# Performance work log

Hardware: AMD Instinct MI355X
Metric: run time of the kernel (lower is better)

Reference implementation:

```python
import jax, jax.numpy as jnp
import numpy as np

NUM_HEADS = 16


def setup_inputs() -> dict:
    key = jax.random.key(0)
    k1, k2, k3 = jax.random.split(key, 3)
    B, L, H = 2, 2048, 1024
    return {
        "key": jax.random.normal(k1, (B, L, H), dtype=jnp.float32),
        "W_ctx": jax.random.normal(k2, (H, H), dtype=jnp.float32) * (1.0 / np.sqrt(H)),
        "b_ctx": jax.random.normal(k3, (H,), dtype=jnp.float32) * 0.01,
    }


def reference(key, W_ctx, b_ctx):
    # Note: the torch module defines q/k/v Linear layers but never calls them
    # in forward(); it reshapes the raw input into heads directly.
    B, L, H = key.shape
    dh = H // NUM_HEADS
    # [B, L, H] -> [B, nh, L, dh]
    x = key.reshape(B, L, NUM_HEADS, dh).transpose(0, 2, 1, 3)
    # QK^T then scale by sqrt(head_dim) (key.shape[-1] after head split)
    scores = jnp.einsum("bhqd,bhkd->bhqk", x, x) * (1.0 / np.float32(np.sqrt(dh)))
    attn = jax.nn.softmax(scores, axis=-1)  # dropout p treated as eval/identity
    ctx = jnp.einsum("bhqk,bhkd->bhqd", attn, x)
    # [B, nh, L, dh] -> [B, L, H]
    ctx = ctx.transpose(0, 2, 1, 3).reshape(B, L, H)
    # context_transform: nn.Linear(H, H, bias=True)
    return ctx @ W_ctx.T + b_ctx
```

## Files before the change

kernel.cpp:

```cpp
#include <hip/hip_runtime.h>
#include <stdint.h>

#define NH     16
#define LSEQ   2048
#define DH     64
#define HDIM   1024
#define BATCH  2

typedef __attribute__((ext_vector_type(8))) short bf16x8;
typedef __attribute__((ext_vector_type(4))) short bf16x4;
typedef __attribute__((ext_vector_type(8))) unsigned short u16x8;
typedef __attribute__((ext_vector_type(4))) float f32x4;

static __device__ inline unsigned short f2bs(float f) {
    union { float f; uint32_t u; } v; v.f = f;
    uint32_t u = v.u;
    return (unsigned short)((u + 0x7FFFu + ((u >> 16) & 1u)) >> 16);
}

#define GLOAD_LDS(gp, lp) \
    __builtin_amdgcn_global_load_lds((const __attribute__((address_space(1))) void*)(gp), \
                                     (__attribute__((address_space(3))) void*)(lp), 16, 0, 0)

#define QK_SCALE 0.42466083f

__global__ __launch_bounds__(256) void prep_kernel(const float* __restrict__ x,
                                                   const float* __restrict__ W,
                                                   unsigned short* __restrict__ xb,
                                                   unsigned short* __restrict__ xt,
                                                   unsigned short* __restrict__ wbt) {
    const int lt = blockIdx.x, bh = blockIdx.y;
    const int bid = bh * 32 + lt;
    const int t = threadIdx.x;

    if (t < 128) {
        const int gid = bid * 128 + t;
        const int n  = gid >> 7;
        const int kc = gid & 127;
        const float* src = W + (size_t)n * 1024 + kc * 8;
        float4 f0 = *(const float4*)(src);
        float4 f1 = *(const float4*)(src + 4);
        u16x8 v;
        v[0]=f2bs(f0.x); v[1]=f2bs(f0.y); v[2]=f2bs(f0.z); v[3]=f2bs(f0.w);
        v[4]=f2bs(f1.x); v[5]=f2bs(f1.y); v[6]=f2bs(f1.z); v[7]=f2bs(f1.w);
        const int nt = n >> 7, rn = n & 127;
        const int kt = kc >> 3, c = kc & 7;
        *(u16x8*)(wbt + (((size_t)nt * 16 + kt) * 128 + rn) * 64 + ((c ^ (rn & 7)) * 8)) = v;
    }

    const int b = bh >> 4, h = bh & 15;
    const int r = t >> 2, cp = t & 3;

    __shared__ __align__(16) unsigned short Sm[64][72];

    const float* src = x + ((size_t)(b * LSEQ + lt * 64 + r)) * HDIM + h * DH + cp * 16;
    float4 f0 = *(const float4*)(src);
    float4 f1 = *(const float4*)(src + 4);
    float4 f2 = *(const float4*)(src + 8);
    float4 f3 = *(const float4*)(src + 12);
    u16x8 lo, hi;
    lo[0]=f2bs(f0.x); lo[1]=f2bs(f0.y); lo[2]=f2bs(f0.z); lo[3]=f2bs(f0.w);
    lo[4]=f2bs(f1.x); lo[5]=f2bs(f1.y); lo[6]=f2bs(f1.z); lo[7]=f2bs(f1.w);
    hi[0]=f2bs(f2.x); hi[1]=f2bs(f2.y); hi[2]=f2bs(f2.z); hi[3]=f2bs(f2.w);
    hi[4]=f2bs(f3.x); hi[5]=f2bs(f3.y); hi[6]=f2bs(f3.z); hi[7]=f2bs(f3.w);
    u16x8 slo, shi;
    slo[0]=f2bs(f0.x*QK_SCALE); slo[1]=f2bs(f0.y*QK_SCALE); slo[2]=f2bs(f0.z*QK_SCALE); slo[3]=f2bs(f0.w*QK_SCALE);
    slo[4]=f2bs(f1.x*QK_SCALE); slo[5]=f2bs(f1.y*QK_SCALE); slo[6]=f2bs(f1.z*QK_SCALE); slo[7]=f2bs(f1.w*QK_SCALE);
    shi[0]=f2bs(f2.x*QK_SCALE); shi[1]=f2bs(f2.y*QK_SCALE); shi[2]=f2bs(f2.z*QK_SCALE); shi[3]=f2bs(f2.w*QK_SCALE);
    shi[4]=f2bs(f3.x*QK_SCALE); shi[5]=f2bs(f3.y*QK_SCALE); shi[6]=f2bs(f3.z*QK_SCALE); shi[7]=f2bs(f3.w*QK_SCALE);

    {
        unsigned short* kt = xb + ((size_t)bid) * 4096;
        const int s  = r >> 4, rla = r & 15;
        const int ks = cp >> 1, q0 = (cp & 1) * 2;
        *(u16x8*)(kt + ((s * 2 + ks) * 64 + q0 * 16 + rla) * 8)       = slo;
        *(u16x8*)(kt + ((s * 2 + ks) * 64 + (q0 + 1) * 16 + rla) * 8) = shi;
    }
    *(u16x8*)&Sm[r][cp * 16]     = lo;
    *(u16x8*)&Sm[r][cp * 16 + 8] = hi;
    __syncthreads();

    {
        const int dt = t >> 6, lane = t & 63;
        const int la = lane & 15, quad = lane >> 4;
        const int sw = (lane >> 2) & 3;
        unsigned short* vt = xt + ((size_t)bid) * 4096;
        unsigned short* row = vt + (dt * 64 + lane) * 16;
        #pragma unroll
        for (int g = 0; g < 4; ++g) {
            ushort4 fr;
            fr.x = Sm[g * 16 + quad * 4 + 0][dt * 16 + la];
            fr.y = Sm[g * 16 + quad * 4 + 1][dt * 16 + la];
            fr.z = Sm[g * 16 + quad * 4 + 2][dt * 16 + la];
            fr.w = Sm[g * 16 + quad * 4 + 3][dt * 16 + la];
            *(ushort4*)(row + ((g ^ sw) * 4)) = fr;
        }
    }
}

__global__ __launch_bounds__(256) void attn_kernel(const unsigned short* __restrict__ xb,
                                                   const unsigned short* __restrict__ xt,
                                                   unsigned short* __restrict__ ctxt) {
    const int bh = blockIdx.x;
    const int qt = blockIdx.y;
    const int tid = threadIdx.x;
    const int w = tid >> 6, lane = tid & 63;
    const int la = lane & 15, quad = lane >> 4;
    const int vsw = (lane >> 2) & 3;

    __shared__ __align__(16) unsigned short KL[2][4096];
    __shared__ __align__(16) unsigned short VL[2][4096];

    const unsigned short* xbh = xb + (size_t)bh * 32 * 4096;
    const unsigned short* xth = xt + (size_t)bh * 32 * 4096;
    const int qbase = qt * 128 + w * 32;

    bf16x8 qf[2][2];
    {
        const unsigned short* qs = xbh + (qbase >> 6) * 4096 + ((qbase >> 4) & 3) * 1024;
        qf[0][0] = *(const bf16x8*)(qs + lane * 8);
        qf[0][1] = *(const bf16x8*)(qs + 512 + lane * 8);
        qf[1][0] = *(const bf16x8*)(qs + 1024 + lane * 8);
        qf[1][1] = *(const bf16x8*)(qs + 1536 + lane * 8);
    }

    const f32x4 fzero = {0.f, 0.f, 0.f, 0.f};
    f32x4 acc0[4], acc1[4];
    #pragma unroll
    for (int j = 0; j < 4; ++j) { acc0[j] = fzero; acc1[j] = fzero; }
    float lp0 = 0.f, lp1 = 0.f;

    const int soff = tid * 16;
    #pragma unroll
    for (int j = 0; j < 2; ++j) {
        const int off = j * 4096 + soff;
        GLOAD_LDS((const char*)xbh + off, (char*)KL[0] + off);
        GLOAD_LDS((const char*)xth + off, (char*)VL[0] + off);
    }
    __syncthreads();

    const char* kp = (const char*)xbh + 8192;
    const char* vp = (const char*)xth + 8192;

    for (int tt = 0; tt < 32; ++tt) {
        if (tt < 31) {
            char* kdst = (char*)KL[(tt + 1) & 1];
            GLOAD_LDS(kp + soff,        kdst + soff);
            GLOAD_LDS(kp + 4096 + soff, kdst + 4096 + soff);
        }

        const unsigned short* kb = KL[tt & 1];
        bf16x4 pf0[4], pf1[4];
        {
            float ls0 = 0.f, ls1 = 0.f;
            #pragma unroll
            for (int kvt = 0; kvt < 4; ++kvt) {
                bf16x8 kf0 = *(const bf16x8*)(kb + (kvt * 2 + 0) * 512 + lane * 8);
                bf16x8 kf1 = *(const bf16x8*)(kb + (kvt * 2 + 1) * 512 + lane * 8);
                f32x4 s0 = fzero, s1 = fzero;
                s0 = __builtin_amdgcn_mfma_f32_16x16x32_bf16(kf0, qf[0][0], s0, 0, 0, 0);
                s0 = __builtin_amdgcn_mfma_f32_16x16x32_bf16(kf1, qf[0][1], s0, 0, 0, 0);
                s1 = __builtin_amdgcn_mfma_f32_16x16x32_bf16(kf0, qf[1][0], s1, 0, 0, 0);
                s1 = __builtin_amdgcn_mfma_f32_16x16x32_bf16(kf1, qf[1][1], s1, 0, 0, 0);

                {
                    float p0 = __builtin_amdgcn_exp2f(s0[0]);
                    float p1 = __builtin_amdgcn_exp2f(s0[1]);
                    float p2 = __builtin_amdgcn_exp2f(s0[2]);
                    float p3 = __builtin_amdgcn_exp2f(s0[3]);
                    ls0 += (p0 + p1) + (p2 + p3);
                    union { uint2 u; bf16x4 v; } cv;
                    cv.u = make_uint2(
                        __builtin_amdgcn_perm(__float_as_uint(p1), __float_as_uint(p0), 0x07060302),
                        __builtin_amdgcn_perm(__float_as_uint(p3), __float_as_uint(p2), 0x07060302));
                    pf0[kvt] = cv.v;
                }
                {
                    float p0 = __builtin_amdgcn_exp2f(s1[0]);
                    float p1 = __builtin_amdgcn_exp2f(s1[1]);
                    float p2 = __builtin_amdgcn_exp2f(s1[2]);
                    float p3 = __builtin_amdgcn_exp2f(s1[3]);
                    ls1 += (p0 + p1) + (p2 + p3);
                    union { uint2 u; bf16x4 v; } cv;
                    cv.u = make_uint2(
                        __builtin_amdgcn_perm(__float_as_uint(p1), __float_as_uint(p0), 0x07060302),
                        __builtin_amdgcn_perm(__float_as_uint(p3), __float_as_uint(p2), 0x07060302));
                    pf1[kvt] = cv.v;
                }
            }
            lp0 += ls0;
            lp1 += ls1;
        }

        __syncthreads();

        if (tt < 31) {
            char* vdst = (char*)VL[(tt + 1) & 1];
            GLOAD_LDS(vp + soff,        vdst + soff);
            GLOAD_LDS(vp + 4096 + soff, vdst + 4096 + soff);
            kp += 8192;
            vp += 8192;
        }

        const unsigned short* vb = VL[tt & 1];
        #pragma unroll
        for (int dt = 0; dt < 4; ++dt) {
            const unsigned short* vrow = vb + (dt * 64 + lane) * 16;
            bf16x4 vf0 = *(const bf16x4*)(vrow + ((0 ^ vsw) * 4));
            bf16x4 vf1 = *(const bf16x4*)(vrow + ((1 ^ vsw) * 4));
            bf16x4 vf2 = *(const bf16x4*)(vrow + ((2 ^ vsw) * 4));
            bf16x4 vf3 = *(const bf16x4*)(vrow + ((3 ^ vsw) * 4));
            f32x4 a0 = acc0[dt], a1 = acc1[dt];
            a0 = __builtin_amdgcn_mfma_f32_16x16x16bf16_1k(vf0, pf0[0], a0, 0, 0, 0);
            a0 = __builtin_amdgcn_mfma_f32_16x16x16bf16_1k(vf1, pf0[1], a0, 0, 0, 0);
            a0 = __builtin_amdgcn_mfma_f32_16x16x16bf16_1k(vf2, pf0[2], a0, 0, 0, 0);
            a0 = __builtin_amdgcn_mfma_f32_16x16x16bf16_1k(vf3, pf0[3], a0, 0, 0, 0);
            a1 = __builtin_amdgcn_mfma_f32_16x16x16bf16_1k(vf0, pf1[0], a1, 0, 0, 0);
            a1 = __builtin_amdgcn_mfma_f32_16x16x16bf16_1k(vf1, pf1[1], a1, 0, 0, 0);
            a1 = __builtin_amdgcn_mfma_f32_16x16x16bf16_1k(vf2, pf1[2], a1, 0, 0, 0);
            a1 = __builtin_amdgcn_mfma_f32_16x16x16bf16_1k(vf3, pf1[3], a1, 0, 0, 0);
            acc0[dt] = a0;
            acc1[dt] = a1;
        }
    }

    const int b = bh >> 4, h = bh & 15;
    const int mt = b * 16 + qt;
    unsigned short* tbase = ctxt + ((size_t)mt * 16 + h) * 128 * 64;
    {
        float l0 = lp0;
        l0 += __shfl_xor(l0, 16);
        l0 += __shfl_xor(l0, 32);
        float l1 = lp1;
        l1 += __shfl_xor(l1, 16);
        l1 += __shfl_xor(l1, 32);
        const float inv0 = 1.0f / l0;
        const float inv1 = 1.0f / l1;

        const int rr0 = w * 32 + la;
        unsigned short* rowp0 = tbase + rr0 * 64 + (quad & 1) * 4;
        #pragma unroll
        for (int dt = 0; dt < 4; ++dt) {
            f32x4 a = acc0[dt];
            const int c = dt * 2 + (quad >> 1);
            *(ushort4*)(rowp0 + ((c ^ (rr0 & 7)) * 8)) =
                make_ushort4(f2bs(a[0] * inv0), f2bs(a[1] * inv0),
                             f2bs(a[2] * inv0), f2bs(a[3] * inv0));
        }
        const int rr1 = w * 32 + 16 + la;
        unsigned short* rowp1 = tbase + rr1 * 64 + (quad & 1) * 4;
        #pragma unroll
        for (int dt = 0; dt < 4; ++dt) {
            f32x4 a = acc1[dt];
            const int c = dt * 2 + (quad >> 1);
            *(ushort4*)(rowp1 + ((c ^ (rr1 & 7)) * 8)) =
                make_ushort4(f2bs(a[0] * inv1), f2bs(a[1] * inv1),
                             f2bs(a[2] * inv1), f2bs(a[3] * inv1));
        }
    }
}

__global__ __launch_bounds__(256) void proj_kernel(const unsigned short* __restrict__ ctxt,
                                                   const unsigned short* __restrict__ wbt,
                                                   const float* __restrict__ bias,
                                                   float* __restrict__ out) {
    const int ntb = blockIdx.x;
    const int mtb = blockIdx.y;
    const int tid = threadIdx.x;
    const int w = tid >> 6, lane = tid & 63;
    const int la = lane & 15, quad = lane >> 4;
    const int wm = (w >> 1) * 64, wn = (w & 1) * 64;

    __shared__ __align__(16) unsigned short As[2][8192];
    __shared__ __align__(16) unsigned short Bs[2][8192];

    const unsigned short* abase = ctxt + (size_t)mtb * 16 * 8192;
    const unsigned short* bbase = wbt  + (size_t)ntb * 16 * 8192;

    const int sw0 = ((quad)     ^ (la & 7)) * 8;
    const int sw1 = ((quad + 4) ^ (la & 7)) * 8;

    const f32x4 fzero = {0.f, 0.f, 0.f, 0.f};
    f32x4 acc[4][4];
    #pragma unroll
    for (int i = 0; i < 4; ++i)
        #pragma unroll
        for (int j = 0; j < 4; ++j) acc[i][j] = fzero;

    #pragma unroll
    for (int j = 0; j < 4; ++j) {
        const int fc = j * 256 + tid;
        GLOAD_LDS((const char*)abase + fc * 16, (char*)As[0] + fc * 16);
        GLOAD_LDS((const char*)bbase + fc * 16, (char*)Bs[0] + fc * 16);
    }
    __syncthreads();

    for (int kt = 0; kt < 16; ++kt) {
        if (kt < 15) {
            const char* asrc = (const char*)(abase + (kt + 1) * 8192);
            const char* bsrc = (const char*)(bbase + (kt + 1) * 8192);
            char* adst = (char*)As[(kt + 1) & 1];
            char* bdst = (char*)Bs[(kt + 1) & 1];
            #pragma unroll
            for (int j = 0; j < 4; ++j) {
                const int fc = j * 256 + tid;
                GLOAD_LDS(asrc + fc * 16, adst + fc * 16);
                GLOAD_LDS(bsrc + fc * 16, bdst + fc * 16);
            }
        }

        const unsigned short* Ab = As[kt & 1];
        const unsigned short* Bb = Bs[kt & 1];
        #pragma unroll
        for (int ks2 = 0; ks2 < 2; ++ks2) {
            const int sw = ks2 ? sw1 : sw0;
            bf16x8 af[4], bfr[4];
            #pragma unroll
            for (int mt = 0; mt < 4; ++mt) af[mt]  = *(const bf16x8*)&Ab[(wm + mt * 16 + la) * 64 + sw];
            #pragma unroll
            for (int nt = 0; nt < 4; ++nt) bfr[nt] = *(const bf16x8*)&Bb[(wn + nt * 16 + la) * 64 + sw];
            #pragma unroll
            for (int mt = 0; mt < 4; ++mt)
                #pragma unroll
                for (int nt = 0; nt < 4; ++nt)
                    acc[mt][nt] = __builtin_amdgcn_mfma_f32_16x16x32_bf16(af[mt], bfr[nt], acc[mt][nt], 0, 0, 0);
        }
        __syncthreads();
    }

    const int m0 = mtb * 128, n0 = ntb * 128;
    #pragma unroll
    for (int nt = 0; nt < 4; ++nt) {
        const int n = n0 + wn + nt * 16 + la;
        const float bv = bias[n];
        #pragma unroll
        for (int mt = 0; mt < 4; ++mt)
            #pragma unroll
            for (int r = 0; r < 4; ++r) {
                const int m = m0 + wm + mt * 16 + quad * 4 + r;
                out[(size_t)m * HDIM + n] = acc[mt][nt][r] + bv;
            }
    }
}

extern "C" void kernel_launch(void* const* d_in, const int* in_sizes, int n_in,
                              void* d_out, int out_size, void* d_ws, size_t ws_size,
                              hipStream_t stream) {
    const float* x    = (const float*)d_in[0];
    const float* W    = (const float*)d_in[1];
    const float* bias = (const float*)d_in[2];
    float* out = (float*)d_out;

    unsigned short* ctxt = (unsigned short*)d_ws;
    unsigned short* xbp  = (unsigned short*)((char*)d_ws + ( 8u << 20));
    unsigned short* xtp  = (unsigned short*)((char*)d_ws + (16u << 20));
    unsigned short* wbt  = (unsigned short*)((char*)d_ws + (24u << 20));

    prep_kernel<<<dim3(32, 32), 256, 0, stream>>>(x, W, xbp, xtp, wbt);
    attn_kernel<<<dim3(32, 16), 256, 0, stream>>>(xbp, xtp, ctxt);
    proj_kernel<<<dim3(8, 32), 256, 0, stream>>>(ctxt, wbt, bias, out);
}
```

Measured before the change: 154.2 us.

## Deepen K/V prefetch to a 4-slot ring and use one barrier per tile

The K/V shared-memory buffers grow from double to quadruple buffering, and loads are now issued two tiles ahead for both K and V. The two __syncthreads per iteration are replaced by a single explicit vmcnt wait and s_barrier. The aim is to hide global-to-LDS latency and cut synchronisation stalls. In exchange, LDS use per block doubles to 64KB, which can lower the number of blocks resident per CU.

```diff
diff --git a/kernel.cpp b/kernel.cpp
--- a/kernel.cpp
+++ b/kernel.cpp
@@ -108,8 +108,8 @@
     const int la = lane & 15, quad = lane >> 4;
     const int vsw = (lane >> 2) & 3;
 
-    __shared__ __align__(16) unsigned short KL[2][4096];
-    __shared__ __align__(16) unsigned short VL[2][4096];
+    __shared__ __align__(16) unsigned short KL[4][4096];
+    __shared__ __align__(16) unsigned short VL[4][4096];
 
     const unsigned short* xbh = xb + (size_t)bh * 32 * 4096;
     const unsigned short* xth = xt + (size_t)bh * 32 * 4096;
@@ -131,25 +131,32 @@
     float lp0 = 0.f, lp1 = 0.f;
 
     const int soff = tid * 16;
+
     #pragma unroll
     for (int j = 0; j < 2; ++j) {
-        const int off = j * 4096 + soff;
-        GLOAD_LDS((const char*)xbh + off, (char*)KL[0] + off);
-        GLOAD_LDS((const char*)xth + off, (char*)VL[0] + off);
-    }
-    __syncthreads();
-
-    const char* kp = (const char*)xbh + 8192;
-    const char* vp = (const char*)xth + 8192;
+        const char* kps = (const char*)xbh + j * 8192;
+        const char* vps = (const char*)xth + j * 8192;
+        GLOAD_LDS(kps + soff,        (char*)KL[j] + soff);
+        GLOAD_LDS(kps + 4096 + soff, (char*)KL[j] + 4096 + soff);
+        GLOAD_LDS(vps + soff,        (char*)VL[j] + soff);
+        GLOAD_LDS(vps + 4096 + soff, (char*)VL[j] + 4096 + soff);
+    }
+    asm volatile("s_waitcnt vmcnt(4)" ::: "memory");
+    __builtin_amdgcn_s_barrier();
 
     for (int tt = 0; tt < 32; ++tt) {
-        if (tt < 31) {
-            char* kdst = (char*)KL[(tt + 1) & 1];
-            GLOAD_LDS(kp + soff,        kdst + soff);
-            GLOAD_LDS(kp + 4096 + soff, kdst + 4096 + soff);
-        }
-
-        const unsigned short* kb = KL[tt & 1];
+        if (tt < 30) {
+            const char* kps = (const char*)xbh + (tt + 2) * 8192;
+            const char* vps = (const char*)xth + (tt + 2) * 8192;
+            char* kdst = (char*)KL[(tt + 2) & 3];
+            char* vdst = (char*)VL[(tt + 2) & 3];
+            GLOAD_LDS(kps + soff,        kdst + soff);
+            GLOAD_LDS(kps + 4096 + soff, kdst + 4096 + soff);
+            GLOAD_LDS(vps + soff,        vdst + soff);
+            GLOAD_LDS(vps + 4096 + soff, vdst + 4096 + soff);
+        }
+
+        const unsigned short* kb = KL[tt & 3];
         bf16x4 pf0[4], pf1[4];
         {
             float ls0 = 0.f, ls1 = 0.f;
@@ -192,17 +199,14 @@
             lp1 += ls1;
         }
 
-        __syncthreads();
-
-        if (tt < 31) {
-            char* vdst = (char*)VL[(tt + 1) & 1];
-            GLOAD_LDS(vp + soff,        vdst + soff);
-            GLOAD_LDS(vp + 4096 + soff, vdst + 4096 + soff);
-            kp += 8192;
-            vp += 8192;
-        }
-
-        const unsigned short* vb = VL[tt & 1];
+        if (tt < 30) {
+            asm volatile("s_waitcnt vmcnt(4)" ::: "memory");
+        } else {
+            asm volatile("s_waitcnt vmcnt(0)" ::: "memory");
+        }
+        __builtin_amdgcn_s_barrier();
+
+        const unsigned short* vb = VL[tt & 3];
         #pragma unroll
         for (int dt = 0; dt < 4; ++dt) {
             const unsigned short* vrow = vb + (dt * 64 + lane) * 16;
```

New measurement: 144.9 us. 6.0% less time.
